# Optimization experiments

Measured on AMD Instinct MI355X. Metric: run time of the kernel, lower is better.

Reference implementation:

```python
import jax, jax.numpy as jnp
import numpy as np

DIM = 640
M_SPATIAL = 100  # 10*10
BATCH = 64
EPS = 1e-5


def setup_inputs() -> dict:
    key = jax.random.key(0)
    kx, = jax.random.split(key, 1)
    x = jax.random.normal(kx, (BATCH, DIM, M_SPATIAL), dtype=jnp.float32)
    # temperature buffer: log(1 / (2 * H * W)) as in BDC.__init__
    t = jnp.log(1.0 / (2.0 * M_SPATIAL) * jnp.ones((1, 1), dtype=jnp.float32))
    return {"x": x, "t": t}


def reference(x, t):
    B, dim, M = x.shape
    # x_pow2 = x @ x^T  -> [B, dim, dim]
    x_pow2 = jnp.einsum('bim,bjm->bij', x, x)
    # I_M.bmm(x_pow2*I) broadcasts diag along rows; (x_pow2*I).bmm(I_M) along cols
    d = jnp.diagonal(x_pow2, axis1=1, axis2=2)  # [B, dim], squared norms
    dcov = d[:, :, None] + d[:, None, :] - 2.0 * x_pow2
    dcov = jnp.clip(dcov, 0.0)
    dcov = jnp.exp(t) * dcov
    dcov = jnp.sqrt(dcov + EPS)
    # double centering: dcov.bmm(I_M) = row sums broadcast, I_M.bmm(dcov) = col sums
    row_mean = jnp.sum(dcov, axis=2, keepdims=True) / dim          # [B, dim, 1]
    col_mean = jnp.sum(dcov, axis=1, keepdims=True) / dim          # [B, 1, dim]
    grand_mean = jnp.sum(dcov, axis=(1, 2), keepdims=True) / (dim * dim)
    bdc = dcov - row_mean - col_mean + grand_mean                   # [B, dim, dim]
    # Triuvec: upper triangle incl. diagonal, row-major order
    iu_r, iu_c = np.triu_indices(dim)
    return bdc[:, iu_r, iu_c]  # [B, dim*(dim+1)//2]
```

## Files before the change

### kernel.cpp

```cpp
#include <hip/hip_runtime.h>
#include <math.h>

#define BATCH 64
#define DIM   640
#define MSP   100
#define TILE  64
#define NT    10
#define NPAIR 55
#define BT    128
#define NT2   5
#define NPAIR2 15
#define NBLK2 960
#define PTRI  205120
#define EPSV  1e-5f

#define WS_D 0
#define WS_S 40960
#define WS_G 81920
#define XB_OFF 327936ull

typedef __attribute__((ext_vector_type(8))) short short8;
typedef __attribute__((ext_vector_type(4))) float f32x4;

__device__ __forceinline__ short f2bf(float f) {
    union { float f; unsigned u; } x; x.f = f;
    unsigned r = x.u + 0x7fffu + ((x.u >> 16) & 1u);
    return (short)(r >> 16);
}
__device__ __forceinline__ float bf2f(short h) {
    union { unsigned u; float f; } x; x.u = ((unsigned)(unsigned short)h) << 16;
    return x.f;
}

template <int NT_>
__device__ __forceinline__ void decode_pairN(int u, int& ti, int& tj) {
    ti = 0;
    while (u >= NT_ - ti) { u -= NT_ - ti; ++ti; }
    tj = ti + u;
}

__device__ __forceinline__ void decode_block128(int bid, int& b, int& ti, int& tj) {
    const int xcd = bid & 7;
    const int idx = bid >> 3;
    b = xcd + 8 * (idx & 7);
    decode_pairN<NT2>(idx >> 3, ti, tj);
}

__device__ __forceinline__ void decode_block64(int bid, int& b, int& ti, int& tj) {
    const int xcd = bid & 7;
    const int idx = bid >> 3;
    b = xcd + 8 * (idx & 7);
    decode_pairN<NT>(idx >> 3, ti, tj);
}

__global__ __launch_bounds__(256) void k_prep(const float* __restrict__ x,
                                              float* __restrict__ ws) {
    short* xb = (short*)((char*)ws + XB_OFF);
    const int t = threadIdx.x;
    const int rr = t >> 4, c = t & 15;
    const int row = blockIdx.x * 16 + rr;
    const int k0 = c * 8;
    const float* src = x + (size_t)row * MSP;

    float v[8];
#pragma unroll
    for (int e = 0; e < 8; ++e) v[e] = 0.f;
    if (k0 <= 88) {
        float4 u0 = *(const float4*)(src + k0);
        float4 u1 = *(const float4*)(src + k0 + 4);
        v[0] = u0.x; v[1] = u0.y; v[2] = u0.z; v[3] = u0.w;
        v[4] = u1.x; v[5] = u1.y; v[6] = u1.z; v[7] = u1.w;
    } else if (k0 == 96) {
        float4 u0 = *(const float4*)(src + 96);
        v[0] = u0.x; v[1] = u0.y; v[2] = u0.z; v[3] = u0.w;
    }

    short8 h; float s = 0.f;
#pragma unroll
    for (int e = 0; e < 8; ++e) {
        short hb = f2bf(v[e]);
        float vr = bf2f(hb);
        s += vr * vr;
        h[e] = hb;
    }
    *(short8*)(xb + (size_t)blockIdx.x * 2048 + c * 128 + rr * 8) = h;

    s += __shfl_xor(s, 1); s += __shfl_xor(s, 2);
    s += __shfl_xor(s, 4); s += __shfl_xor(s, 8);
    if (c == 0) { ws[WS_D + row] = s; ws[WS_S + row] = 0.f; }
    if (blockIdx.x == 0 && t < BATCH) ws[WS_G + t] = 0.f;
}

__global__ __launch_bounds__(256) void k_sums(const float* __restrict__ tsc,
                                              float* __restrict__ ws) {
    __shared__ float sRow[BT];
    __shared__ float sCol[BT];

    int b, ti, tj;
    decode_block128(blockIdx.x, b, ti, tj);
    const int i0 = ti * BT, j0 = tj * BT;
    const int tid = threadIdx.x;
    const short* xb = (const short*)((const char*)ws + XB_OFF);

    if (tid < BT) { sRow[tid] = 0.f; sCol[tid] = 0.f; }

    const int wave = tid >> 6, lane = tid & 63;
    const int lm = lane & 15, lq = lane >> 4;
    const int r0 = (wave >> 1) * 64, c0 = (wave & 1) * 64;

    const short* pa = xb + (size_t)(b * 40 + ((i0 + r0) >> 4)) * 2048 + lq * 128 + lm * 8;
    const short* pb = xb + (size_t)(b * 40 + ((j0 + c0) >> 4)) * 2048 + lq * 128 + lm * 8;

    f32x4 acc[4][4] = {};
#pragma unroll
    for (int ks = 0; ks < 4; ++ks) {
        short8 af[4], bf[4];
#pragma unroll
        for (int m = 0; m < 4; ++m) af[m] = *(const short8*)(pa + m * 2048 + ks * 512);
#pragma unroll
        for (int n = 0; n < 4; ++n) bf[n] = *(const short8*)(pb + n * 2048 + ks * 512);
#pragma unroll
        for (int m = 0; m < 4; ++m)
#pragma unroll
            for (int n = 0; n < 4; ++n)
                acc[m][n] = __builtin_amdgcn_mfma_f32_16x16x32_bf16(af[m], bf[n], acc[m][n], 0, 0, 0);
    }

    const float scale = expf(tsc[0]);
    const float* dn = ws + WS_D + b * DIM;
    float dj[4];
#pragma unroll
    for (int n = 0; n < 4; ++n) dj[n] = dn[j0 + c0 + 16 * n + lm];

    float rp[4][4] = {}, cp[4] = {};
#pragma unroll
    for (int m = 0; m < 4; ++m) {
        float di_[4];
#pragma unroll
        for (int r = 0; r < 4; ++r) di_[r] = dn[i0 + r0 + 16 * m + 4 * lq + r];
#pragma unroll
        for (int n = 0; n < 4; ++n)
#pragma unroll
            for (int p = 0; p < 4; ++p) {
                float v = __builtin_amdgcn_sqrtf(
                    fmaf(scale, fmaxf(fmaf(-2.f, acc[m][n][p], di_[p] + dj[n]), 0.f), EPSV));
                rp[m][p] += v; cp[n] += v;
            }
    }

    __syncthreads();
#pragma unroll
    for (int m = 0; m < 4; ++m)
#pragma unroll
        for (int p = 0; p < 4; ++p) {
            float v = rp[m][p];
            v += __shfl_xor(v, 1); v += __shfl_xor(v, 2);
            v += __shfl_xor(v, 4); v += __shfl_xor(v, 8);
            if (lm == 0) atomicAdd(&sRow[r0 + 16 * m + 4 * lq + p], v);
        }
#pragma unroll
    for (int n = 0; n < 4; ++n) {
        float v = cp[n];
        v += __shfl_xor(v, 16); v += __shfl_xor(v, 32);
        if (lq == 0) atomicAdd(&sCol[c0 + 16 * n + lm], v);
    }
    __syncthreads();

    float* S = ws + WS_S + b * DIM;
    if (tid < BT) {
        atomicAdd(&S[i0 + tid], sRow[tid]);
        if (ti != tj) atomicAdd(&S[j0 + tid], sCol[tid]);
        float gg = sRow[tid];
        gg += __shfl_xor(gg, 1);  gg += __shfl_xor(gg, 2);  gg += __shfl_xor(gg, 4);
        gg += __shfl_xor(gg, 8);  gg += __shfl_xor(gg, 16); gg += __shfl_xor(gg, 32);
        if (lane == 0) atomicAdd(&ws[WS_G + b], (ti == tj ? 1.f : 2.f) * gg);
    }
}

__global__ __launch_bounds__(256) void k_write(const float* __restrict__ tsc,
                                               const float* __restrict__ ws,
                                               float* __restrict__ out) {
    int b, ti, tj;
    decode_block64(blockIdx.x, b, ti, tj);
    const int i0 = ti * TILE, j0 = tj * TILE;
    const int tid = threadIdx.x;
    const short* xb = (const short*)((const char*)ws + XB_OFF);

    const int wave = tid >> 6, lane = tid & 63;
    const int lm = lane & 15, lq = lane >> 4;
    const int wr = wave >> 1, wc = wave & 1;
    const int r0 = wr * 32, c0 = wc * 32;

    const bool diag = (ti == tj);
    if (diag && wr > wc) return;
    const bool pred = diag && (wr == wc);

    const short* pa = xb + (size_t)(b * 40 + ((i0 + r0) >> 4)) * 2048 + lq * 128 + lm * 8;
    const short* pb = xb + (size_t)(b * 40 + ((j0 + c0) >> 4)) * 2048 + lq * 128 + lm * 8;

    f32x4 acc[2][2] = {};
#pragma unroll
    for (int ks = 0; ks < 4; ++ks) {
        short8 a0 = *(const short8*)(pa + ks * 512);
        short8 a1 = *(const short8*)(pa + 2048 + ks * 512);
        short8 b0 = *(const short8*)(pb + ks * 512);
        short8 b1 = *(const short8*)(pb + 2048 + ks * 512);
        acc[0][0] = __builtin_amdgcn_mfma_f32_16x16x32_bf16(a0, b0, acc[0][0], 0, 0, 0);
        acc[0][1] = __builtin_amdgcn_mfma_f32_16x16x32_bf16(a0, b1, acc[0][1], 0, 0, 0);
        acc[1][0] = __builtin_amdgcn_mfma_f32_16x16x32_bf16(a1, b0, acc[1][0], 0, 0, 0);
        acc[1][1] = __builtin_amdgcn_mfma_f32_16x16x32_bf16(a1, b1, acc[1][1], 0, 0, 0);
    }

    const float scale = expf(tsc[0]);
    const float inv = 1.f / (float)DIM;
    const float g = ws[WS_G + b] * (inv * inv);
    const float* S  = ws + WS_S + b * DIM;
    const float* dn = ws + WS_D + b * DIM;

    float di[2][4], ai[2][4]; int ib[2][4];
#pragma unroll
    for (int a = 0; a < 2; ++a)
#pragma unroll
        for (int r = 0; r < 4; ++r) {
            int i = i0 + r0 + 16 * a + 4 * lq + r;
            di[a][r] = dn[i];
            ai[a][r] = g - S[i] * inv;
            ib[a][r] = i * DIM - (i * (i - 1)) / 2 - i;
        }
    float dj[2], bj[2]; int jj[2];
#pragma unroll
    for (int bb = 0; bb < 2; ++bb) {
        int j = j0 + c0 + 16 * bb + lm;
        jj[bb] = j; dj[bb] = dn[j]; bj[bb] = -S[j] * inv;
    }

    float* outb = out + (size_t)b * PTRI;
#pragma unroll
    for (int a = 0; a < 2; ++a) {
        const int ibase = i0 + r0 + 16 * a + 4 * lq;
#pragma unroll
        for (int bb = 0; bb < 2; ++bb)
#pragma unroll
            for (int p = 0; p < 2; ++p) {
                const int r = 2 * p;
                float d0 = di[a][r]     + dj[bb];
                float d1 = di[a][r + 1] + dj[bb];
                float v0 = __builtin_amdgcn_sqrtf(
                    fmaf(scale, fmaxf(fmaf(-2.f, acc[a][bb][r],     d0), 0.f), EPSV));
                float v1 = __builtin_amdgcn_sqrtf(
                    fmaf(scale, fmaxf(fmaf(-2.f, acc[a][bb][r + 1], d1), 0.f), EPSV));
                if (!pred || jj[bb] >= ibase + r)
                    outb[ib[a][r]     + jj[bb]] = v0 + ai[a][r]     + bj[bb];
                if (!pred || jj[bb] >= ibase + r + 1)
                    outb[ib[a][r + 1] + jj[bb]] = v1 + ai[a][r + 1] + bj[bb];
            }
    }
}

extern "C" void kernel_launch(void* const* d_in, const int* in_sizes, int n_in,
                              void* d_out, int out_size, void* d_ws, size_t ws_size,
                              hipStream_t stream) {
    const float* x = (const float*)d_in[0];
    const float* t = (const float*)d_in[1];
    float* out = (float*)d_out;
    float* ws  = (float*)d_ws;

    k_prep <<<dim3(BATCH * DIM / 16), 256, 0, stream>>>(x, ws);
    k_sums <<<dim3(NBLK2),            256, 0, stream>>>(t, ws);
    k_write<<<dim3(NPAIR * BATCH),    256, 0, stream>>>(t, ws, out);
}
```

Measured before the change: 114.0 us.

## Fuse bf16 prep into sums kernel and replace atomics with partial-sum buffers

```diff
diff --git a/kernel.cpp b/kernel.cpp
--- a/kernel.cpp
+++ b/kernel.cpp
@@ -14,10 +14,10 @@
 #define PTRI  205120
 #define EPSV  1e-5f
 
-#define WS_D 0
-#define WS_S 40960
-#define WS_G 81920
-#define XB_OFF 327936ull
+#define WS_D  0
+#define WS_SP 40960
+#define WS_GP 245760
+#define XB_OFF 987136ull
 
 typedef __attribute__((ext_vector_type(8))) short short8;
 typedef __attribute__((ext_vector_type(4))) float f32x4;
@@ -39,11 +39,13 @@
     tj = ti + u;
 }
 
-__device__ __forceinline__ void decode_block128(int bid, int& b, int& ti, int& tj) {
+__device__ __forceinline__ void decode_block128(int bid, int& b, int& u,
+                                                int& ti, int& tj) {
     const int xcd = bid & 7;
     const int idx = bid >> 3;
     b = xcd + 8 * (idx & 7);
-    decode_pairN<NT2>(idx >> 3, ti, tj);
+    u = idx >> 3;
+    decode_pairN<NT2>(u, ti, tj);
 }
 
 __device__ __forceinline__ void decode_block64(int bid, int& b, int& ti, int& tj) {
@@ -53,72 +55,84 @@
     decode_pairN<NT>(idx >> 3, ti, tj);
 }
 
-__global__ __launch_bounds__(256) void k_prep(const float* __restrict__ x,
+__global__ __launch_bounds__(256) void k_sums(const float* __restrict__ x,
+                                              const float* __restrict__ tsc,
                                               float* __restrict__ ws) {
-    short* xb = (short*)((char*)ws + XB_OFF);
-    const int t = threadIdx.x;
-    const int rr = t >> 4, c = t & 15;
-    const int row = blockIdx.x * 16 + rr;
-    const int k0 = c * 8;
-    const float* src = x + (size_t)row * MSP;
-
-    float v[8];
-#pragma unroll
-    for (int e = 0; e < 8; ++e) v[e] = 0.f;
-    if (k0 <= 88) {
-        float4 u0 = *(const float4*)(src + k0);
-        float4 u1 = *(const float4*)(src + k0 + 4);
-        v[0] = u0.x; v[1] = u0.y; v[2] = u0.z; v[3] = u0.w;
-        v[4] = u1.x; v[5] = u1.y; v[6] = u1.z; v[7] = u1.w;
-    } else if (k0 == 96) {
-        float4 u0 = *(const float4*)(src + 96);
-        v[0] = u0.x; v[1] = u0.y; v[2] = u0.z; v[3] = u0.w;
-    }
-
-    short8 h; float s = 0.f;
-#pragma unroll
-    for (int e = 0; e < 8; ++e) {
-        short hb = f2bf(v[e]);
-        float vr = bf2f(hb);
-        s += vr * vr;
-        h[e] = hb;
-    }
-    *(short8*)(xb + (size_t)blockIdx.x * 2048 + c * 128 + rr * 8) = h;
-
-    s += __shfl_xor(s, 1); s += __shfl_xor(s, 2);
-    s += __shfl_xor(s, 4); s += __shfl_xor(s, 8);
-    if (c == 0) { ws[WS_D + row] = s; ws[WS_S + row] = 0.f; }
-    if (blockIdx.x == 0 && t < BATCH) ws[WS_G + t] = 0.f;
-}
-
-__global__ __launch_bounds__(256) void k_sums(const float* __restrict__ tsc,
-                                              float* __restrict__ ws) {
+    __shared__ __align__(16) short lxb[16 * 2048];
+    __shared__ float nrm[256];
     __shared__ float sRow[BT];
     __shared__ float sCol[BT];
 
-    int b, ti, tj;
-    decode_block128(blockIdx.x, b, ti, tj);
+    int b, u, ti, tj;
+    decode_block128(blockIdx.x, b, u, ti, tj);
     const int i0 = ti * BT, j0 = tj * BT;
     const int tid = threadIdx.x;
-    const short* xb = (const short*)((const char*)ws + XB_OFF);
+    const bool diag = (ti == tj);
+    short* xbg = (short*)((char*)ws + XB_OFF);
 
     if (tid < BT) { sRow[tid] = 0.f; sCol[tid] = 0.f; }
+
+    {
+        const int rr = tid >> 4, c = tid & 15;
+        const int k0 = c * 8;
+        const int npan = diag ? 8 : 16;
+        for (int pp = 0; pp < npan; ++pp) {
+            const int rowBase = (pp < 8) ? (i0 + pp * 16) : (j0 + (pp - 8) * 16);
+            const int row = rowBase + rr;
+            const float* src = x + ((size_t)b * DIM + row) * MSP;
+
+            float v[8];
+#pragma unroll
+            for (int e = 0; e < 8; ++e) v[e] = 0.f;
+            if (k0 <= 88) {
+                float4 u0 = *(const float4*)(src + k0);
+                float4 u1 = *(const float4*)(src + k0 + 4);
+                v[0] = u0.x; v[1] = u0.y; v[2] = u0.z; v[3] = u0.w;
+                v[4] = u1.x; v[5] = u1.y; v[6] = u1.z; v[7] = u1.w;
+            } else if (k0 == 96) {
+                float4 u0 = *(const float4*)(src + 96);
+                v[0] = u0.x; v[1] = u0.y; v[2] = u0.z; v[3] = u0.w;
+            }
+
+            short8 h; float s = 0.f;
+#pragma unroll
+            for (int e = 0; e < 8; ++e) {
+                short hb = f2bf(v[e]);
+                float vr = bf2f(hb);
+                s += vr * vr;
+                h[e] = hb;
+            }
+            *(short8*)&lxb[pp * 2048 + c * 128 + rr * 8] = h;
+            if (diag)
+                *(short8*)(xbg + (size_t)(b * 40 + (i0 >> 4) + pp) * 2048
+                           + c * 128 + rr * 8) = h;
+
+            s += __shfl_xor(s, 1); s += __shfl_xor(s, 2);
+            s += __shfl_xor(s, 4); s += __shfl_xor(s, 8);
+            if (c == 0) {
+                nrm[pp * 16 + rr] = s;
+                if (diag) ws[WS_D + b * DIM + row] = s;
+            }
+        }
+    }
+    __syncthreads();
 
     const int wave = tid >> 6, lane = tid & 63;
     const int lm = lane & 15, lq = lane >> 4;
     const int r0 = (wave >> 1) * 64, c0 = (wave & 1) * 64;
-
-    const short* pa = xb + (size_t)(b * 40 + ((i0 + r0) >> 4)) * 2048 + lq * 128 + lm * 8;
-    const short* pb = xb + (size_t)(b * 40 + ((j0 + c0) >> 4)) * 2048 + lq * 128 + lm * 8;
+    const int aP0 = r0 >> 4;
+    const int bP0 = (diag ? 0 : 8) + (c0 >> 4);
 
     f32x4 acc[4][4] = {};
 #pragma unroll
     for (int ks = 0; ks < 4; ++ks) {
         short8 af[4], bf[4];
 #pragma unroll
-        for (int m = 0; m < 4; ++m) af[m] = *(const short8*)(pa + m * 2048 + ks * 512);
-#pragma unroll
-        for (int n = 0; n < 4; ++n) bf[n] = *(const short8*)(pb + n * 2048 + ks * 512);
+        for (int m = 0; m < 4; ++m)
+            af[m] = *(const short8*)&lxb[(aP0 + m) * 2048 + ks * 512 + lq * 128 + lm * 8];
+#pragma unroll
+        for (int n = 0; n < 4; ++n)
+            bf[n] = *(const short8*)&lxb[(bP0 + n) * 2048 + ks * 512 + lq * 128 + lm * 8];
 #pragma unroll
         for (int m = 0; m < 4; ++m)
 #pragma unroll
@@ -127,17 +141,17 @@
     }
 
     const float scale = expf(tsc[0]);
-    const float* dn = ws + WS_D + b * DIM;
+    const int nOff = diag ? 0 : 128;
     float dj[4];
 #pragma unroll
-    for (int n = 0; n < 4; ++n) dj[n] = dn[j0 + c0 + 16 * n + lm];
+    for (int n = 0; n < 4; ++n) dj[n] = nrm[nOff + c0 + 16 * n + lm];
 
     float rp[4][4] = {}, cp[4] = {};
 #pragma unroll
     for (int m = 0; m < 4; ++m) {
         float di_[4];
 #pragma unroll
-        for (int r = 0; r < 4; ++r) di_[r] = dn[i0 + r0 + 16 * m + 4 * lq + r];
+        for (int r = 0; r < 4; ++r) di_[r] = nrm[r0 + 16 * m + 4 * lq + r];
 #pragma unroll
         for (int n = 0; n < 4; ++n)
 #pragma unroll
@@ -148,7 +162,6 @@
             }
     }
 
-    __syncthreads();
 #pragma unroll
     for (int m = 0; m < 4; ++m)
 #pragma unroll
@@ -166,25 +179,51 @@
     }
     __syncthreads();
 
-    float* S = ws + WS_S + b * DIM;
+    float* sp = ws + WS_SP;
     if (tid < BT) {
-        atomicAdd(&S[i0 + tid], sRow[tid]);
-        if (ti != tj) atomicAdd(&S[j0 + tid], sCol[tid]);
-        float gg = sRow[tid];
+        sp[((b * 5 + ti) * 5 + tj) * 128 + tid] = sRow[tid];
+        if (!diag)
+            sp[((b * 5 + tj) * 5 + ti) * 128 + tid] = sCol[tid];
+    }
+    if (tid < 64) {
+        float gg = sRow[tid] + sRow[tid + 64];
         gg += __shfl_xor(gg, 1);  gg += __shfl_xor(gg, 2);  gg += __shfl_xor(gg, 4);
         gg += __shfl_xor(gg, 8);  gg += __shfl_xor(gg, 16); gg += __shfl_xor(gg, 32);
-        if (lane == 0) atomicAdd(&ws[WS_G + b], (ti == tj ? 1.f : 2.f) * gg);
+        if (tid == 0) ws[WS_GP + b * 15 + u] = (diag ? 1.f : 2.f) * gg;
     }
 }
 
 __global__ __launch_bounds__(256) void k_write(const float* __restrict__ tsc,
                                                const float* __restrict__ ws,
                                                float* __restrict__ out) {
+    __shared__ float Sl[128];
+    __shared__ float gsh;
+
     int b, ti, tj;
     decode_block64(blockIdx.x, b, ti, tj);
     const int i0 = ti * TILE, j0 = tj * TILE;
     const int tid = threadIdx.x;
     const short* xb = (const short*)((const char*)ws + XB_OFF);
+
+    {
+        const float* sp = ws + WS_SP;
+        if (tid < 64) {
+            const float* p = sp + (size_t)((b * 5 + (ti >> 1)) * 5) * 128
+                             + ((ti & 1) << 6) + tid;
+            Sl[tid] = p[0] + p[128] + p[256] + p[384] + p[512];
+        } else if (tid < 128) {
+            const float* p = sp + (size_t)((b * 5 + (tj >> 1)) * 5) * 128
+                             + ((tj & 1) << 6) + (tid - 64);
+            Sl[tid] = p[0] + p[128] + p[256] + p[384] + p[512];
+        } else if (tid < 192) {
+            const int l = tid & 63;
+            float gv = (l < 15) ? ws[WS_GP + b * 15 + l] : 0.f;
+            gv += __shfl_xor(gv, 1); gv += __shfl_xor(gv, 2);
+            gv += __shfl_xor(gv, 4); gv += __shfl_xor(gv, 8);
+            if (l == 0) gsh = gv;
+        }
+    }
+    __syncthreads();
 
     const int wave = tid >> 6, lane = tid & 63;
     const int lm = lane & 15, lq = lane >> 4;
@@ -213,8 +252,7 @@
 
     const float scale = expf(tsc[0]);
     const float inv = 1.f / (float)DIM;
-    const float g = ws[WS_G + b] * (inv * inv);
-    const float* S  = ws + WS_S + b * DIM;
+    const float g = gsh * (inv * inv);
     const float* dn = ws + WS_D + b * DIM;
 
     float di[2][4], ai[2][4]; int ib[2][4];
@@ -223,15 +261,17 @@
 #pragma unroll
         for (int r = 0; r < 4; ++r) {
             int i = i0 + r0 + 16 * a + 4 * lq + r;
+            int il = r0 + 16 * a + 4 * lq + r;
             di[a][r] = dn[i];
-            ai[a][r] = g - S[i] * inv;
+            ai[a][r] = g - Sl[il] * inv;
             ib[a][r] = i * DIM - (i * (i - 1)) / 2 - i;
         }
     float dj[2], bj[2]; int jj[2];
 #pragma unroll
     for (int bb = 0; bb < 2; ++bb) {
         int j = j0 + c0 + 16 * bb + lm;
-        jj[bb] = j; dj[bb] = dn[j]; bj[bb] = -S[j] * inv;
+        jj[bb] = j; dj[bb] = dn[j];
+        bj[bb] = -Sl[64 + c0 + 16 * bb + lm] * inv;
     }
 
     float* outb = out + (size_t)b * PTRI;
@@ -265,7 +305,6 @@
     float* out = (float*)d_out;
     float* ws  = (float*)d_ws;
 
-    k_prep <<<dim3(BATCH * DIM / 16), 256, 0, stream>>>(x, ws);
-    k_sums <<<dim3(NBLK2),            256, 0, stream>>>(t, ws);
-    k_write<<<dim3(NPAIR * BATCH),    256, 0, stream>>>(t, ws, out);
-}
+    k_sums <<<dim3(NBLK2),         256, 0, stream>>>(x, t, ws);
+    k_write<<<dim3(NPAIR * BATCH), 256, 0, stream>>>(t, ws, out);
+}
```

Result: slower. 123.1 us (+8.0%).
